# Optimization experiments

Hardware: AMD Instinct MI355X
Metric: run time of the kernel (lower is better)

## Reference

```python
import jax, jax.numpy as jnp
import numpy as np

B, H, S, DK = 4, 16, 2048, 128


def setup_inputs() -> dict:
    key = jax.random.key(0)
    kq, kk, kv = jax.random.split(key, 3)
    q = jax.random.normal(kq, (B, H, S, DK), dtype=jnp.float32)
    k = jax.random.normal(kk, (B, H, S, DK), dtype=jnp.float32)
    v = jax.random.normal(kv, (B, H, S, DK), dtype=jnp.float32)
    # causal mask, broadcastable over batch and heads; 0 => masked
    mask = jnp.tril(jnp.ones((S, S), dtype=jnp.int32))[None, None, :, :]
    return {"q": q, "k": k, "v": v, "mask": mask}


def reference(q, k, v, mask):
    d_k = q.shape[-1]
    scale = 1.0 / jnp.sqrt(jnp.float32(d_k))
    # [B,H,S,S] scores
    attn = jnp.einsum("bhqd,bhkd->bhqk", q, k) * scale
    attn = jnp.where(mask == 0, jnp.float32(-1e9), attn)
    attn = jax.nn.softmax(attn, axis=-1)
    # dropout is identity in eval mode (reference is deterministic)
    output = jnp.einsum("bhqk,bhkd->bhqd", attn, v)
    return (output, attn)
```

## Files before the change

### kernel.cpp

```cpp
#include <hip/hip_runtime.h>
#include <hip/hip_bf16.h>


#define BDIM 4
#define HDIM 16
#define SDIM 2048
#define DDIM 128
#define MT 64
#define NT 64
#define QP 136
#define KP 136
#define VP 72
#define PP 72
#define P32P 68

typedef __attribute__((ext_vector_type(8))) short bf16x8;
typedef __attribute__((ext_vector_type(4))) float f32x4;

__device__ __forceinline__ unsigned short f2bf(float f) {
    unsigned int u = __float_as_uint(f);
    u += 0x7FFFu + ((u >> 16) & 1u);
    return (unsigned short)(u >> 16);
}

__global__ __launch_bounds__(256, 2)
void sdpa_kernel(const float* __restrict__ q, const float* __restrict__ k,
                 const float* __restrict__ v, float* __restrict__ outO,
                 float* __restrict__ outP)
{
    __shared__ __align__(16) unsigned short q_s[MT * QP];
    __shared__ __align__(16) unsigned short k_s[NT * KP];
    __shared__ __align__(16) unsigned short vt_s[DDIM * VP];
    __shared__ __align__(16) unsigned short p_s[4][16 * PP];
    __shared__ __align__(16) float p32_s[4][16 * P32P];

    const int tid  = threadIdx.x;
    const int lane = tid & 63;
    const int w    = tid >> 6;
    const int qn   = lane >> 4;
    const int ln   = lane & 15;

    const int bidx = blockIdx.x;
    const int bh   = bidx >> 5;
    const int qt   = 31 - (bidx & 31);
    const int i0   = qt * MT;
    const int jt_d = i0 >> 6;
    const int iw0  = i0 + 16 * w;

    const float scale = 0.08838834764831845f;

    const float* qb = q + (size_t)bh * SDIM * DDIM;
    const float* kb = k + (size_t)bh * SDIM * DDIM;
    const float* vb = v + (size_t)bh * SDIM * DDIM;

    {
        const int c0 = i0 + MT;
        const int count4 = (SDIM - c0) >> 2;
        if (count4 > 0) {
            const float4 z4 = make_float4(0.f, 0.f, 0.f, 0.f);
            for (int row = 0; row < MT; ++row) {
                float4* dst = (float4*)(outP + (size_t)(bh * SDIM + i0 + row) * SDIM + c0);
                for (int c = tid; c < count4; c += 256) dst[c] = z4;
            }
        }
    }

    for (int it = 0; it < 8; ++it) {
        int linear = it * 256 + tid;
        int row = linear >> 5;
        int c4  = linear & 31;
        float4 f4 = *(const float4*)(qb + (size_t)(i0 + row) * DDIM + 4 * c4);
        ushort4 h;
        h.x = f2bf(f4.x); h.y = f2bf(f4.y); h.z = f2bf(f4.z); h.w = f2bf(f4.w);
        *(ushort4*)&q_s[row * QP + 4 * c4] = h;
    }
    __syncthreads();

    bf16x8 afr[4];
#pragma unroll
    for (int ks = 0; ks < 4; ++ks)
        afr[ks] = *(const bf16x8*)&q_s[(16 * w + ln) * QP + 8 * qn + 32 * ks];

    auto stageK = [&](int j0) {
        for (int it = 0; it < 8; ++it) {
            int linear = it * 256 + tid;
            int row = linear >> 5, c4 = linear & 31;
            float4 f4 = *(const float4*)(kb + (size_t)(j0 + row) * DDIM + 4 * c4);
            ushort4 h;
            h.x = f2bf(f4.x); h.y = f2bf(f4.y); h.z = f2bf(f4.z); h.w = f2bf(f4.w);
            *(ushort4*)&k_s[row * KP + 4 * c4] = h;
        }
    };

    auto computeS = [&](f32x4* sfr) {
#pragma unroll
        for (int nb = 0; nb < 4; ++nb) {
            f32x4 acc = {0.f, 0.f, 0.f, 0.f};
#pragma unroll
            for (int ks = 0; ks < 4; ++ks) {
                bf16x8 bfr = *(const bf16x8*)&k_s[(16 * nb + ln) * KP + 8 * qn + 32 * ks];
                acc = __builtin_amdgcn_mfma_f32_16x16x32_bf16(afr[ks], bfr, acc, 0, 0, 0);
            }
            sfr[nb] = acc;
        }
    };

    float mrow[4], lrow[4];
#pragma unroll
    for (int r = 0; r < 4; ++r) { mrow[r] = -1e30f; lrow[r] = 0.f; }

    for (int jt = 0; jt <= jt_d; ++jt) {
        const int j0 = jt * NT;
        __syncthreads();
        stageK(j0);
        __syncthreads();

        f32x4 sfr[4];
        computeS(sfr);
        const bool needmask = (jt == jt_d);

#pragma unroll
        for (int r = 0; r < 4; ++r) {
            const int irow = iw0 + 4 * qn + r;
            float tmax = -1e30f;
            float sv[4];
#pragma unroll
            for (int nb = 0; nb < 4; ++nb) {
                float s = sfr[nb][r] * scale;
                int j = j0 + 16 * nb + ln;
                if (needmask && j > irow) s = -1e30f;
                sv[nb] = s;
                tmax = fmaxf(tmax, s);
            }
            for (int off = 1; off < 16; off <<= 1)
                tmax = fmaxf(tmax, __shfl_xor(tmax, off, 64));
            const float mnew = fmaxf(mrow[r], tmax);
            float sum = 0.f;
#pragma unroll
            for (int nb = 0; nb < 4; ++nb) sum += __expf(sv[nb] - mnew);
            for (int off = 1; off < 16; off <<= 1)
                sum += __shfl_xor(sum, off, 64);
            lrow[r] = lrow[r] * __expf(mrow[r] - mnew) + sum;
            mrow[r] = mnew;
        }
    }

    float invl[4];
#pragma unroll
    for (int r = 0; r < 4; ++r) invl[r] = 1.0f / lrow[r];

    f32x4 oacc[8];
#pragma unroll
    for (int db = 0; db < 8; ++db) oacc[db] = {0.f, 0.f, 0.f, 0.f};

    for (int jt = 0; jt <= jt_d; ++jt) {
        const int j0 = jt * NT;
        __syncthreads();
        stageK(j0);
        for (int it = 0; it < 8; ++it) {
            int linear = it * 256 + tid;
            int d = linear & 127, jg = linear >> 7;
            ushort4 h;
            h.x = f2bf(vb[(size_t)(j0 + 4 * jg + 0) * DDIM + d]);
            h.y = f2bf(vb[(size_t)(j0 + 4 * jg + 1) * DDIM + d]);
            h.z = f2bf(vb[(size_t)(j0 + 4 * jg + 2) * DDIM + d]);
            h.w = f2bf(vb[(size_t)(j0 + 4 * jg + 3) * DDIM + d]);
            *(ushort4*)&vt_s[d * VP + 4 * jg] = h;
        }
        __syncthreads();

        f32x4 sfr[4];
        computeS(sfr);
        const bool needmask = (jt == jt_d);

#pragma unroll
        for (int nb = 0; nb < 4; ++nb) {
#pragma unroll
            for (int r = 0; r < 4; ++r) {
                const int irow = iw0 + 4 * qn + r;
                const int j = j0 + 16 * nb + ln;
                float s = sfr[nb][r] * scale;
                float p = (needmask && j > irow) ? 0.f
                          : __expf(s - mrow[r]) * invl[r];
                const int m = 4 * qn + r;
                p32_s[w][m * P32P + 16 * nb + ln] = p;
                p_s[w][m * PP + 16 * nb + ln] = f2bf(p);
            }
        }
        __syncthreads();

#pragma unroll
        for (int rep = 0; rep < 4; ++rep) {
            int idx = rep * 64 + lane;
            int row = idx >> 4;
            int c4  = idx & 15;
            *(float4*)(outP + (size_t)(bh * SDIM + iw0 + row) * SDIM + j0 + 4 * c4) =
                *(const float4*)&p32_s[w][row * P32P + 4 * c4];
        }

        bf16x8 pfr[2];
#pragma unroll
        for (int ks = 0; ks < 2; ++ks)
            pfr[ks] = *(const bf16x8*)&p_s[w][ln * PP + 8 * qn + 32 * ks];
#pragma unroll
        for (int db = 0; db < 8; ++db) {
#pragma unroll
            for (int ks = 0; ks < 2; ++ks) {
                bf16x8 bfr = *(const bf16x8*)&vt_s[(16 * db + ln) * VP + 8 * qn + 32 * ks];
                oacc[db] = __builtin_amdgcn_mfma_f32_16x16x32_bf16(pfr[ks], bfr, oacc[db], 0, 0, 0);
            }
        }
    }

#pragma unroll
    for (int db = 0; db < 8; ++db) {
#pragma unroll
        for (int r = 0; r < 4; ++r) {
            outO[(size_t)(bh * SDIM + iw0 + 4 * qn + r) * DDIM + 16 * db + ln] = oacc[db][r];
        }
    }
}

extern "C" void kernel_launch(void* const* d_in, const int* in_sizes, int n_in,
                              void* d_out, int out_size, void* d_ws, size_t ws_size,
                              hipStream_t stream) {
    const float* q = (const float*)d_in[0];
    const float* k = (const float*)d_in[1];
    const float* v = (const float*)d_in[2];
    float* outO = (float*)d_out;
    float* outP = outO + (size_t)BDIM * HDIM * SDIM * DDIM;

    dim3 grid(BDIM * HDIM * (SDIM / MT));
    dim3 block(256);
    sdpa_kernel<<<grid, block, 0, stream>>>(q, k, v, outO, outP);
}
```

Measured before the change: 1.756 ms.

## Double-buffer K via register prefetch, shrink LDS, swizzle V, nontemporal stores

Prefetches the next K tile into registers while the current tile's MFMA runs, alternating between two LDS buffers. The Q, V and P buffers are merged into one shared buffer, and the bf16 P copy is dropped by converting from the fp32 LDS tile, so LDS shrinks and launch bounds can rise to 3 blocks per CU. It also remaps block indices, XOR-swizzles the transposed V layout to avoid bank conflicts, and uses nontemporal stores for the zero-fill and outputs. The risks are higher register pressure under the tighter launch bound and the correctness of the buffer reuse, since the barrier after writing the P tile was removed.

```diff
diff --git a/kernel.cpp b/kernel.cpp
--- a/kernel.cpp
+++ b/kernel.cpp
@@ -11,7 +11,6 @@
 #define QP 136
 #define KP 136
 #define VP 72
-#define PP 72
 #define P32P 68
 
 typedef __attribute__((ext_vector_type(8))) short bf16x8;
@@ -23,15 +22,13 @@
     return (unsigned short)(u >> 16);
 }
 
-__global__ __launch_bounds__(256, 2)
+__global__ __launch_bounds__(256, 3)
 void sdpa_kernel(const float* __restrict__ q, const float* __restrict__ k,
                  const float* __restrict__ v, float* __restrict__ outO,
                  float* __restrict__ outP)
 {
-    __shared__ __align__(16) unsigned short q_s[MT * QP];
     __shared__ __align__(16) unsigned short k_s[NT * KP];
-    __shared__ __align__(16) unsigned short vt_s[DDIM * VP];
-    __shared__ __align__(16) unsigned short p_s[4][16 * PP];
+    __shared__ __align__(16) unsigned short uv_s[DDIM * VP];
     __shared__ __align__(16) float p32_s[4][16 * P32P];
 
     const int tid  = threadIdx.x;
@@ -40,7 +37,8 @@
     const int qn   = lane >> 4;
     const int ln   = lane & 15;
 
-    const int bidx = blockIdx.x;
+    const int bid  = blockIdx.x;
+    const int bidx = (bid & 7) * 256 + (bid >> 3);
     const int bh   = bidx >> 5;
     const int qt   = 31 - (bidx & 31);
     const int i0   = qt * MT;
@@ -57,10 +55,11 @@
         const int c0 = i0 + MT;
         const int count4 = (SDIM - c0) >> 2;
         if (count4 > 0) {
-            const float4 z4 = make_float4(0.f, 0.f, 0.f, 0.f);
+            const f32x4 z4 = {0.f, 0.f, 0.f, 0.f};
             for (int row = 0; row < MT; ++row) {
-                float4* dst = (float4*)(outP + (size_t)(bh * SDIM + i0 + row) * SDIM + c0);
-                for (int c = tid; c < count4; c += 256) dst[c] = z4;
+                f32x4* dst = (f32x4*)(outP + (size_t)(bh * SDIM + i0 + row) * SDIM + c0);
+                for (int c = tid; c < count4; c += 256)
+                    __builtin_nontemporal_store(z4, dst + c);
             }
         }
     }
@@ -72,33 +71,41 @@
         float4 f4 = *(const float4*)(qb + (size_t)(i0 + row) * DDIM + 4 * c4);
         ushort4 h;
         h.x = f2bf(f4.x); h.y = f2bf(f4.y); h.z = f2bf(f4.z); h.w = f2bf(f4.w);
-        *(ushort4*)&q_s[row * QP + 4 * c4] = h;
+        *(ushort4*)&uv_s[row * QP + 4 * c4] = h;
     }
     __syncthreads();
 
     bf16x8 afr[4];
 #pragma unroll
     for (int ks = 0; ks < 4; ++ks)
-        afr[ks] = *(const bf16x8*)&q_s[(16 * w + ln) * QP + 8 * qn + 32 * ks];
-
-    auto stageK = [&](int j0) {
+        afr[ks] = *(const bf16x8*)&uv_s[(16 * w + ln) * QP + 8 * qn + 32 * ks];
+
+    auto stageK_regs = [&](float4* kst, int j0) {
+#pragma unroll
         for (int it = 0; it < 8; ++it) {
             int linear = it * 256 + tid;
             int row = linear >> 5, c4 = linear & 31;
-            float4 f4 = *(const float4*)(kb + (size_t)(j0 + row) * DDIM + 4 * c4);
+            kst[it] = *(const float4*)(kb + (size_t)(j0 + row) * DDIM + 4 * c4);
+        }
+    };
+    auto writeK_lds = [&](unsigned short* dst, const float4* kst) {
+#pragma unroll
+        for (int it = 0; it < 8; ++it) {
+            int linear = it * 256 + tid;
+            int row = linear >> 5, c4 = linear & 31;
             ushort4 h;
-            h.x = f2bf(f4.x); h.y = f2bf(f4.y); h.z = f2bf(f4.z); h.w = f2bf(f4.w);
-            *(ushort4*)&k_s[row * KP + 4 * c4] = h;
+            h.x = f2bf(kst[it].x); h.y = f2bf(kst[it].y);
+            h.z = f2bf(kst[it].z); h.w = f2bf(kst[it].w);
+            *(ushort4*)&dst[row * KP + 4 * c4] = h;
         }
     };
-
-    auto computeS = [&](f32x4* sfr) {
+    auto computeS = [&](const unsigned short* ks_, f32x4* sfr) {
 #pragma unroll
         for (int nb = 0; nb < 4; ++nb) {
             f32x4 acc = {0.f, 0.f, 0.f, 0.f};
 #pragma unroll
             for (int ks = 0; ks < 4; ++ks) {
-                bf16x8 bfr = *(const bf16x8*)&k_s[(16 * nb + ln) * KP + 8 * qn + 32 * ks];
+                bf16x8 bfr = *(const bf16x8*)&ks_[(16 * nb + ln) * KP + 8 * qn + 32 * ks];
                 acc = __builtin_amdgcn_mfma_f32_16x16x32_bf16(afr[ks], bfr, acc, 0, 0, 0);
             }
             sfr[nb] = acc;
@@ -108,17 +115,28 @@
     float mrow[4], lrow[4];
 #pragma unroll
     for (int r = 0; r < 4; ++r) { mrow[r] = -1e30f; lrow[r] = 0.f; }
+
+    {
+        float4 kst0[8];
+        stageK_regs(kst0, 0);
+        writeK_lds(k_s, kst0);
+    }
+    __syncthreads();
 
     for (int jt = 0; jt <= jt_d; ++jt) {
         const int j0 = jt * NT;
-        __syncthreads();
-        stageK(j0);
-        __syncthreads();
+        const unsigned short* cur = (jt & 1) ? uv_s : k_s;
+        unsigned short* nxt = (jt & 1) ? k_s : uv_s;
+
+        float4 kst1[8];
+        if (jt < jt_d) stageK_regs(kst1, j0 + NT);
 
         f32x4 sfr[4];
-        computeS(sfr);
+        computeS(cur, sfr);
+
+        if (jt < jt_d) writeK_lds(nxt, kst1);
+
         const bool needmask = (jt == jt_d);
-
 #pragma unroll
         for (int r = 0; r < 4; ++r) {
             const int irow = iw0 + 4 * qn + r;
@@ -143,6 +161,7 @@
             lrow[r] = lrow[r] * __expf(mrow[r] - mnew) + sum;
             mrow[r] = mnew;
         }
+        __syncthreads();
     }
 
     float invl[4];
@@ -152,11 +171,15 @@
     f32x4 oacc[8];
 #pragma unroll
     for (int db = 0; db < 8; ++db) oacc[db] = {0.f, 0.f, 0.f, 0.f};
+
+    float4 kst[8];
+    stageK_regs(kst, 0);
 
     for (int jt = 0; jt <= jt_d; ++jt) {
         const int j0 = jt * NT;
         __syncthreads();
-        stageK(j0);
+        writeK_lds(k_s, kst);
+#pragma unroll
         for (int it = 0; it < 8; ++it) {
             int linear = it * 256 + tid;
             int d = linear & 127, jg = linear >> 7;
@@ -165,12 +188,13 @@
             h.y = f2bf(vb[(size_t)(j0 + 4 * jg + 1) * DDIM + d]);
             h.z = f2bf(vb[(size_t)(j0 + 4 * jg + 2) * DDIM + d]);
             h.w = f2bf(vb[(size_t)(j0 + 4 * jg + 3) * DDIM + d]);
-            *(ushort4*)&vt_s[d * VP + 4 * jg] = h;
+            int col = (4 * jg) ^ (((d >> 3) & 7) << 3);
+            *(ushort4*)&uv_s[d * VP + col] = h;
         }
         __syncthreads();
 
         f32x4 sfr[4];
-        computeS(sfr);
+        computeS(k_s, sfr);
         const bool needmask = (jt == jt_d);
 
 #pragma unroll
@@ -182,31 +206,43 @@
                 float s = sfr[nb][r] * scale;
                 float p = (needmask && j > irow) ? 0.f
                           : __expf(s - mrow[r]) * invl[r];
-                const int m = 4 * qn + r;
-                p32_s[w][m * P32P + 16 * nb + ln] = p;
-                p_s[w][m * PP + 16 * nb + ln] = f2bf(p);
-            }
-        }
-        __syncthreads();
+                p32_s[w][(4 * qn + r) * P32P + 16 * nb + ln] = p;
+            }
+        }
 
 #pragma unroll
         for (int rep = 0; rep < 4; ++rep) {
             int idx = rep * 64 + lane;
             int row = idx >> 4;
             int c4  = idx & 15;
-            *(float4*)(outP + (size_t)(bh * SDIM + iw0 + row) * SDIM + j0 + 4 * c4) =
-                *(const float4*)&p32_s[w][row * P32P + 4 * c4];
+            f32x4 val = *(const f32x4*)&p32_s[w][row * P32P + 4 * c4];
+            __builtin_nontemporal_store(val,
+                (f32x4*)(outP + (size_t)(bh * SDIM + iw0 + row) * SDIM + j0 + 4 * c4));
         }
 
         bf16x8 pfr[2];
 #pragma unroll
-        for (int ks = 0; ks < 2; ++ks)
-            pfr[ks] = *(const bf16x8*)&p_s[w][ln * PP + 8 * qn + 32 * ks];
+        for (int ks = 0; ks < 2; ++ks) {
+            const float* pp = &p32_s[w][ln * P32P + 8 * qn + 32 * ks];
+            f32x4 lo = *(const f32x4*)pp;
+            f32x4 hi = *(const f32x4*)(pp + 4);
+            bf16x8 t;
+            t[0] = (short)f2bf(lo[0]); t[1] = (short)f2bf(lo[1]);
+            t[2] = (short)f2bf(lo[2]); t[3] = (short)f2bf(lo[3]);
+            t[4] = (short)f2bf(hi[0]); t[5] = (short)f2bf(hi[1]);
+            t[6] = (short)f2bf(hi[2]); t[7] = (short)f2bf(hi[3]);
+            pfr[ks] = t;
+        }
+
+        if (jt < jt_d) stageK_regs(kst, j0 + NT);
+
 #pragma unroll
         for (int db = 0; db < 8; ++db) {
 #pragma unroll
             for (int ks = 0; ks < 2; ++ks) {
-                bf16x8 bfr = *(const bf16x8*)&vt_s[(16 * db + ln) * VP + 8 * qn + 32 * ks];
+                int vrow = 16 * db + ln;
+                int col = (8 * qn + 32 * ks) ^ (((vrow >> 3) & 7) << 3);
+                bf16x8 bfr = *(const bf16x8*)&uv_s[vrow * VP + col];
                 oacc[db] = __builtin_amdgcn_mfma_f32_16x16x32_bf16(pfr[ks], bfr, oacc[db], 0, 0, 0);
             }
         }
@@ -216,7 +252,8 @@
     for (int db = 0; db < 8; ++db) {
 #pragma unroll
         for (int r = 0; r < 4; ++r) {
-            outO[(size_t)(bh * SDIM + iw0 + 4 * qn + r) * DDIM + 16 * db + ln] = oacc[db][r];
+            __builtin_nontemporal_store(oacc[db][r],
+                outO + (size_t)(bh * SDIM + iw0 + 4 * qn + r) * DDIM + 16 * db + ln);
         }
     }
 }
```

Result: faster. 1.538 ms (-12.4%).
